# Kernel optimization log

Measured on AMD Instinct MI355X. Metric: run time of the kernel, lower is better.

Reference implementation:

```python
import jax, jax.numpy as jnp
import numpy as np

N = 20000   # nodes
E = 320000  # edges
NE = 2000   # entities
H = 4       # attention heads
D = 128     # hidden_dim (per-head out feats)
K = 10      # knn k


def _gat(h, src, dst, W, al, ar, Wr, relu):
    # h: [N, Fin]; W: [H*D, Fin]; al/ar: [H, D]; Wr: [H*D, Fin]
    feat = (h @ W.T).reshape(N, H, D)                      # [N,H,D]
    el = jnp.sum(feat * al[None], axis=-1)                 # [N,H]
    er = jnp.sum(feat * ar[None], axis=-1)                 # [N,H]
    e = jax.nn.leaky_relu(el[src] + er[dst], 0.2)          # [E,H]
    emax = jax.ops.segment_max(e, dst, num_segments=N)
    emax = jnp.where(jnp.isfinite(emax), emax, 0.0)
    a = jnp.exp(e - emax[dst])                             # [E,H]
    asum = jax.ops.segment_sum(a, dst, num_segments=N)
    asum = jnp.where(asum > 0, asum, 1.0)
    alpha = a / asum[dst]                                  # edge softmax over incoming edges
    msg = alpha[:, :, None] * feat[src]                    # [E,H,D]
    rst = jax.ops.segment_sum(msg, dst, num_segments=N)    # [N,H,D]
    rst = rst + (h @ Wr.T).reshape(N, H, D)                # residual
    if relu:
        rst = jax.nn.relu(rst)
    return rst


def _mlp2(x, W1, b1, W2, b2):
    return jax.nn.sigmoid(jax.nn.relu(x @ W1.T + b1) @ W2.T + b2)


def setup_inputs() -> dict:
    key = jax.random.key(0)
    ks = jax.random.split(key, 32)
    f32 = jnp.float32
    p = lambda i, s: (jax.random.normal(ks[i], s, dtype=f32) * 0.05)
    inp = {
        'position': jax.random.normal(ks[0], (N, 2), dtype=f32),
        'w_embed': jax.random.normal(ks[1], (N, 126), dtype=f32),
        'src': jax.random.randint(ks[2], (E,), 0, N),
        'dst': jax.random.randint(ks[3], (E,), 0, N),
        'entity': jax.random.randint(ks[4], (N,), 0, NE),
        # GAT layer 1 (in=128)
        'W1': p(5, (H * D, 128)), 'al1': p(6, (H, D)), 'ar1': p(7, (H, D)), 'Wr1': p(8, (H * D, 128)),
        # GAT layer 2 (in=512)
        'W2': p(9, (H * D, H * D)), 'al2': p(10, (H, D)), 'ar2': p(11, (H, D)), 'Wr2': p(12, (H * D, H * D)),
        # GAT layer 3 (in=512)
        'W3': p(13, (H * D, H * D)), 'al3': p(14, (H, D)), 'ar3': p(15, (H, D)), 'Wr3': p(16, (H * D, H * D)),
        # w_group_mlp
        'Wg1': p(17, (D, D)), 'bg1': p(18, (D,)), 'Wg2': p(19, (1, D)), 'bg2': p(20, (1,)),
        # entity_linear
        'We': p(21, (D, D)), 'be': p(22, (D,)),
        # entity_link_mlp
        'Wl1': p(23, (D, D)), 'bl1': p(24, (D,)), 'Wl2': p(25, (1, D)), 'bl2': p(26, (1,)),
        # entity_classify
        'Wc': p(27, (4, D)), 'bc': p(28, (4,)),
    }
    return inp


def reference(position, w_embed, src, dst, entity,
              W1, al1, ar1, Wr1, W2, al2, ar2, Wr2, W3, al3, ar3, Wr3,
              Wg1, bg1, Wg2, bg2, We, be, Wl1, bl1, Wl2, bl2, Wc, bc):
    h = jnp.concatenate([position, w_embed], axis=1)        # [N,128]
    h = _gat(h, src, dst, W1, al1, ar1, Wr1, True).reshape(N, H * D)
    h = _gat(h, src, dst, W2, al2, ar2, Wr2, True).reshape(N, H * D)
    h = _gat(h, src, dst, W3, al3, ar3, Wr3, False).mean(axis=1)  # [N,D]

    # pairwise group score over edges
    groups_score = _mlp2(jnp.abs(h[src] - h[dst]), Wg1, bg1, Wg2, bg2).squeeze(-1)  # [E]

    # per-entity segment reduce
    ent_sum = jax.ops.segment_sum(h, entity, num_segments=NE)            # [NE,D]
    entity_states = ent_sum @ We.T + be                                  # [NE,D]
    pos_sum = jax.ops.segment_sum(position, entity, num_segments=NE)     # [NE,2]
    cnt = jax.ops.segment_sum(jnp.ones((N,), jnp.float32), entity, num_segments=NE)
    entity_positions = pos_sum / jnp.maximum(cnt, 1.0)[:, None]          # [NE,2]

    # knn graph on entity centroids (k=10, includes self like dgl.knn_graph)
    d2 = jnp.sum((entity_positions[:, None, :] - entity_positions[None, :, :]) ** 2, axis=-1)  # [NE,NE]
    _, knn_idx = jax.lax.top_k(-d2, K)                                   # [NE,K]
    src_e = knn_idx.reshape(-1)                                          # [NE*K]
    dst_e = jnp.repeat(jnp.arange(NE), K)
    entity_link_score = _mlp2(jnp.abs(entity_states[src_e] - entity_states[dst_e]),
                              Wl1, bl1, Wl2, bl2).squeeze(-1)            # [NE*K]

    entity_class = jax.nn.sigmoid(entity_states @ Wc.T + bc)             # [NE,4]
    return (groups_score, entity_class, entity_positions, entity_link_score)
```

## Files before the change

### kernel.cpp

```cpp
#include <hip/hip_runtime.h>
#include <math.h>

#define N_NODES 20000
#define N_EDGES 320000
#define NENT    2000
#define KNN_K   10

typedef __attribute__((ext_vector_type(4))) float f32x4;
typedef __attribute__((ext_vector_type(8))) short bf16x8;
typedef __attribute__((ext_vector_type(8))) unsigned short u16x8;
typedef __attribute__((ext_vector_type(4))) unsigned short u16x4;

__device__ __forceinline__ unsigned short f2bf(float f) {
  union { float f; unsigned u; } v; v.f = f;
  unsigned r = v.u + 0x7fffu + ((v.u >> 16) & 1u);
  return (unsigned short)(r >> 16);
}
__device__ __forceinline__ float bf2f(unsigned short u) {
  union { unsigned u; float f; } v; v.u = ((unsigned)u) << 16;
  return v.f;
}
__device__ __forceinline__ float sigmoidf(float x) {
  return 1.f / (1.f + __expf(-x));
}
__device__ __forceinline__ void gload_lds16(const unsigned short* g, unsigned short* lds) {
  __builtin_amdgcn_global_load_lds(
      (const __attribute__((address_space(1))) unsigned int*)g,
      (__attribute__((address_space(3))) unsigned int*)lds, 16, 0, 0);
}

__global__ void k_build_h0(const float* __restrict__ pos, const float* __restrict__ wemb,
                           unsigned short* __restrict__ h0) {
  int i = blockIdx.x * blockDim.x + threadIdx.x;
  if (i >= N_NODES * 128) return;
  int n = i >> 7, c = i & 127;
  float v = (c < 2) ? pos[n * 2 + c] : wemb[n * 126 + (c - 2)];
  h0[i] = f2bf(v);
}

__global__ void k_f2bf(const float* __restrict__ in, unsigned short* __restrict__ out, int n) {
  int i = blockIdx.x * blockDim.x + threadIdx.x;
  if (i * 4 >= n) return;
  f32x4 v = *(const f32x4*)(in + i * 4);
  u16x4 o;
  o[0] = f2bf(v[0]); o[1] = f2bf(v[1]); o[2] = f2bf(v[2]); o[3] = f2bf(v[3]);
  *(u16x4*)(out + i * 4) = o;
}

__global__ __launch_bounds__(256) void k_gemm_bt(
    const unsigned short* __restrict__ A, const unsigned short* __restrict__ B,
    unsigned short* __restrict__ C, int M, int Nc, int K) {
  __shared__ __align__(16) unsigned short As[128 * 64];
  __shared__ __align__(16) unsigned short Bs[128 * 64];
  const int bm = blockIdx.x * 128, bn = blockIdx.y * 128;
  const int t = threadIdx.x;
  const int l = t & 63, w = t >> 6;
  const int wr = w >> 1, wc = w & 1;
  f32x4 acc[4][4];
#pragma unroll
  for (int m = 0; m < 4; ++m)
#pragma unroll
    for (int n = 0; n < 4; ++n) acc[m][n] = (f32x4){0.f, 0.f, 0.f, 0.f};

  for (int kb = 0; kb < K; kb += 64) {
    __syncthreads();
#pragma unroll
    for (int i = 0; i < 4; ++i) {
      int c = t + 256 * i;
      int row = c >> 3, cc = c & 7;
      int scc = cc ^ (row & 7);
      int ar = bm + row; if (ar > M - 1) ar = M - 1;
      gload_lds16(A + (size_t)ar * K + kb + scc * 8, &As[(size_t)(w * 64 + 256 * i) * 8]);
      gload_lds16(B + (size_t)(bn + row) * K + kb + scc * 8,
                  &Bs[(size_t)(w * 64 + 256 * i) * 8]);
    }
    __syncthreads();
#pragma unroll
    for (int kk = 0; kk < 2; ++kk) {
      bf16x8 af[4], bfr[4];
#pragma unroll
      for (int m = 0; m < 4; ++m) {
        int row = wr * 64 + m * 16 + (l & 15);
        int g = (kk * 4 + (l >> 4)) ^ (row & 7);
        af[m] = *(const bf16x8*)&As[row * 64 + g * 8];
      }
#pragma unroll
      for (int n = 0; n < 4; ++n) {
        int row = wc * 64 + n * 16 + (l & 15);
        int g = (kk * 4 + (l >> 4)) ^ (row & 7);
        bfr[n] = *(const bf16x8*)&Bs[row * 64 + g * 8];
      }
#pragma unroll
      for (int m = 0; m < 4; ++m)
#pragma unroll
        for (int n = 0; n < 4; ++n)
          acc[m][n] = __builtin_amdgcn_mfma_f32_16x16x32_bf16(af[m], bfr[n], acc[m][n], 0, 0, 0);
    }
  }
#pragma unroll
  for (int m = 0; m < 4; ++m) {
    int r0 = bm + wr * 64 + m * 16 + ((l >> 4) << 2);
#pragma unroll
    for (int n = 0; n < 4; ++n) {
      int c0 = bn + wc * 64 + n * 16 + (l & 15);
#pragma unroll
      for (int r = 0; r < 4; ++r) {
        int row = r0 + r;
        if (row < M) C[(size_t)row * Nc + c0] = f2bf(acc[m][n][r]);
      }
    }
  }
}

__global__ void k_el_er(const unsigned short* __restrict__ feat, int fstride,
                        const float* __restrict__ al, const float* __restrict__ ar,
                        float* __restrict__ el, float* __restrict__ er) {
  int wid = (blockIdx.x * blockDim.x + threadIdx.x) >> 6;
  if (wid >= N_NODES) return;
  int l = threadIdx.x & 63;
  int g = l >> 4, q = l & 15;
  u16x8 fv = *(const u16x8*)(feat + (size_t)wid * fstride + l * 8);
  const float* alp = al + g * 128 + q * 8;
  const float* arp = ar + g * 128 + q * 8;
  float sl = 0.f, sr = 0.f;
#pragma unroll
  for (int j = 0; j < 8; ++j) { float f = bf2f(fv[j]); sl += f * alp[j]; sr += f * arp[j]; }
#pragma unroll
  for (int d = 1; d < 16; d <<= 1) { sl += __shfl_xor(sl, d); sr += __shfl_xor(sr, d); }
  if (q == 0) { el[wid * 4 + g] = sl; er[wid * 4 + g] = sr; }
}

__global__ void k_hist(const int* __restrict__ dst, int* __restrict__ indeg) {
  int e = blockIdx.x * blockDim.x + threadIdx.x;
  if (e < N_EDGES) atomicAdd(&indeg[dst[e]], 1);
}

__global__ __launch_bounds__(1024) void k_scan_fast(const int* __restrict__ indeg,
                                                    int* __restrict__ indptr,
                                                    int* __restrict__ cursor) {
  __shared__ int wsum[16];
  const int t = threadIdx.x;
  const int l = t & 63, w = t >> 6;
  const int CH = 20;
  int base = t * CH;
  int vals[CH];
  int s = 0;
#pragma unroll
  for (int i = 0; i < CH; ++i) {
    int idx = base + i;
    int v = (idx < N_NODES) ? indeg[idx] : 0;
    vals[i] = v;
    s += v;
  }
  int ss = s;
#pragma unroll
  for (int d = 1; d < 64; d <<= 1) { int o = __shfl_up(ss, d); if (l >= d) ss += o; }
  if (l == 63) wsum[w] = ss;
  __syncthreads();
  if (t < 16) {
    int v = wsum[t];
#pragma unroll
    for (int d = 1; d < 16; d <<= 1) { int o = __shfl_up(v, d); if (t >= d) v += o; }
    wsum[t] = v;
  }
  __syncthreads();
  int run = ((w > 0) ? wsum[w - 1] : 0) + ss - s;
  if (t == 0) indptr[0] = 0;
#pragma unroll
  for (int i = 0; i < CH; ++i) {
    int idx = base + i;
    if (idx < N_NODES) {
      cursor[idx] = run;
      run += vals[i];
      indptr[idx + 1] = run;
    }
  }
}

__global__ void k_scatter(const int* __restrict__ src, const int* __restrict__ dst,
                          int* __restrict__ cursor, int* __restrict__ csr_src) {
  int e = blockIdx.x * blockDim.x + threadIdx.x;
  if (e < N_EDGES) {
    int p = atomicAdd(&cursor[dst[e]], 1);
    csr_src[p] = src[e];
  }
}

template <bool FINAL>
__global__ void k_gat_agg(const unsigned short* __restrict__ feat,
                          const unsigned short* __restrict__ hres, int fstride,
                          const float* __restrict__ el, const float* __restrict__ er,
                          const int* __restrict__ indptr, const int* __restrict__ csr_src,
                          unsigned short* __restrict__ hnext, float* __restrict__ h3,
                          unsigned short* __restrict__ h3b) {
  int wid = (blockIdx.x * blockDim.x + threadIdx.x) >> 6;
  if (wid >= N_NODES) return;
  int l = threadIdx.x & 63;
  int g = l >> 4;
  int beg = indptr[wid], end = indptr[wid + 1];
  f32x4 er4 = *(const f32x4*)(er + wid * 4);
  const float NI = -__builtin_inff();
  f32x4 mx = (f32x4){NI, NI, NI, NI};
  for (int j = beg + l; j < end; j += 64) {
    int s = csr_src[j];
    f32x4 el4 = *(const f32x4*)(el + s * 4);
#pragma unroll
    for (int h = 0; h < 4; ++h) {
      float v = el4[h] + er4[h];
      v = (v >= 0.f) ? v : 0.2f * v;
      mx[h] = fmaxf(mx[h], v);
    }
  }
#pragma unroll
  for (int d = 1; d < 64; d <<= 1) {
#pragma unroll
    for (int h = 0; h < 4; ++h) mx[h] = fmaxf(mx[h], __shfl_xor(mx[h], d));
  }
  float m_g = mx[g];
  float er_g = er4[g];
  float asum = 0.f;
  float acc[8];
#pragma unroll
  for (int j2 = 0; j2 < 8; ++j2) acc[j2] = 0.f;
  const unsigned short* fbase = feat + l * 8;
  int j = beg;
  for (; j + 4 <= end; j += 4) {
    int s0 = csr_src[j + 0], s1 = csr_src[j + 1];
    int s2 = csr_src[j + 2], s3 = csr_src[j + 3];
    float q0 = el[s0 * 4 + g], q1 = el[s1 * 4 + g];
    float q2 = el[s2 * 4 + g], q3 = el[s3 * 4 + g];
    u16x8 f0 = *(const u16x8*)(fbase + (size_t)s0 * fstride);
    u16x8 f1 = *(const u16x8*)(fbase + (size_t)s1 * fstride);
    u16x8 f2 = *(const u16x8*)(fbase + (size_t)s2 * fstride);
    u16x8 f3 = *(const u16x8*)(fbase + (size_t)s3 * fstride);
    float e0 = q0 + er_g; e0 = (e0 >= 0.f) ? e0 : 0.2f * e0;
    float e1 = q1 + er_g; e1 = (e1 >= 0.f) ? e1 : 0.2f * e1;
    float e2 = q2 + er_g; e2 = (e2 >= 0.f) ? e2 : 0.2f * e2;
    float e3 = q3 + er_g; e3 = (e3 >= 0.f) ? e3 : 0.2f * e3;
    float p0 = __expf(e0 - m_g), p1 = __expf(e1 - m_g);
    float p2 = __expf(e2 - m_g), p3 = __expf(e3 - m_g);
    asum += (p0 + p1) + (p2 + p3);
#pragma unroll
    for (int k = 0; k < 8; ++k)
      acc[k] += p0 * bf2f(f0[k]) + p1 * bf2f(f1[k]) + p2 * bf2f(f2[k]) + p3 * bf2f(f3[k]);
  }
  for (; j < end; ++j) {
    int s = csr_src[j];
    float ev = el[s * 4 + g] + er_g;
    ev = (ev >= 0.f) ? ev : 0.2f * ev;
    float p = __expf(ev - m_g);
    asum += p;
    u16x8 fv = *(const u16x8*)(fbase + (size_t)s * fstride);
#pragma unroll
    for (int k = 0; k < 8; ++k) acc[k] += p * bf2f(fv[k]);
  }
  float inv = (end > beg) ? 1.f / asum : 1.f;
  u16x8 hv = *(const u16x8*)(hres + (size_t)wid * fstride + l * 8);
  float o[8];
#pragma unroll
  for (int k = 0; k < 8; ++k) o[k] = acc[k] * inv + bf2f(hv[k]);
  if constexpr (!FINAL) {
    u16x8 ob;
#pragma unroll
    for (int k = 0; k < 8; ++k) ob[k] = f2bf(fmaxf(o[k], 0.f));
    *(u16x8*)(hnext + (size_t)wid * 512 + l * 8) = ob;
  } else {
#pragma unroll
    for (int k = 0; k < 8; ++k) {
      float v = o[k];
      v += __shfl_xor(v, 16);
      v += __shfl_xor(v, 32);
      o[k] = v * 0.25f;
    }
    if (g == 0) {
      f32x4 o0 = (f32x4){o[0], o[1], o[2], o[3]};
      f32x4 o1 = (f32x4){o[4], o[5], o[6], o[7]};
      *(f32x4*)(h3 + (size_t)wid * 128 + l * 8) = o0;
      *(f32x4*)(h3 + (size_t)wid * 128 + l * 8 + 4) = o1;
      u16x8 hb;
#pragma unroll
      for (int k = 0; k < 8; ++k) hb[k] = f2bf(o[k]);
      *(u16x8*)(h3b + (size_t)wid * 128 + l * 8) = hb;
    }
  }
}

template <int MODE>
__global__ __launch_bounds__(256) void k_pair_mlp(
    const unsigned short* __restrict__ X, const int* __restrict__ ia,
    const int* __restrict__ ib, const unsigned short* __restrict__ Wb,
    const float* __restrict__ b1, const float* __restrict__ W2,
    const float* __restrict__ b2, float* __restrict__ out, int npairs) {
  __shared__ __align__(16) unsigned short Xs[4][32 * 128];
  const int t = threadIdx.x;
  const int l = t & 63, w = t >> 6;
  unsigned short* xs = Xs[w];
  const int base = (blockIdx.x * 4 + w) * 32;
  {
    int e = base + (l >> 1);
    if (e >= npairs) e = npairs - 1;
    int sa, sb;
    if (MODE == 0) { sa = ia[e]; sb = ib[e]; }
    else           { sa = ia[e]; sb = e / KNN_K; }
    int hf = l & 1, el = l >> 1;
    const unsigned short* pa = X + (size_t)sa * 128 + hf * 64;
    const unsigned short* pb = X + (size_t)sb * 128 + hf * 64;
#pragma unroll
    for (int c = 0; c < 8; ++c) {
      u16x8 av = *(const u16x8*)(pa + c * 8);
      u16x8 bv = *(const u16x8*)(pb + c * 8);
      u16x8 xv;
#pragma unroll
      for (int j = 0; j < 8; ++j) xv[j] = f2bf(fabsf(bf2f(av[j]) - bf2f(bv[j])));
      int sg = (hf * 8 + c) ^ (el & 15);
      *(u16x8*)&xs[el * 128 + sg * 8] = xv;
    }
  }
  __syncthreads();
  bf16x8 af[2][4];
#pragma unroll
  for (int m = 0; m < 2; ++m)
#pragma unroll
    for (int kk = 0; kk < 4; ++kk) {
      int row = m * 16 + (l & 15);
      int sg = (kk * 4 + (l >> 4)) ^ (row & 15);
      af[m][kk] = *(const bf16x8*)&xs[row * 128 + sg * 8];
    }
  const size_t wlane = (size_t)(l & 15) * 128 + (l >> 4) * 8;
  bf16x8 bcur[4], bnext[4];
#pragma unroll
  for (int kk = 0; kk < 4; ++kk)
    bcur[kk] = *(const bf16x8*)(Wb + wlane + kk * 32);
  float part[2][4];
#pragma unroll
  for (int m = 0; m < 2; ++m)
#pragma unroll
    for (int r = 0; r < 4; ++r) part[m][r] = 0.f;
#pragma unroll
  for (int n = 0; n < 8; ++n) {
    if (n < 7) {
#pragma unroll
      for (int kk = 0; kk < 4; ++kk)
        bnext[kk] = *(const bf16x8*)(Wb + wlane + (size_t)(n + 1) * 2048 + kk * 32);
    }
    f32x4 acc0 = (f32x4){0.f, 0.f, 0.f, 0.f};
    f32x4 acc1 = (f32x4){0.f, 0.f, 0.f, 0.f};
#pragma unroll
    for (int kk = 0; kk < 4; ++kk) {
      acc0 = __builtin_amdgcn_mfma_f32_16x16x32_bf16(af[0][kk], bcur[kk], acc0, 0, 0, 0);
      acc1 = __builtin_amdgcn_mfma_f32_16x16x32_bf16(af[1][kk], bcur[kk], acc1, 0, 0, 0);
    }
    int col = n * 16 + (l & 15);
    float bb = b1[col], w2v = W2[col];
#pragma unroll
    for (int r = 0; r < 4; ++r) {
      part[0][r] += fmaxf(acc0[r] + bb, 0.f) * w2v;
      part[1][r] += fmaxf(acc1[r] + bb, 0.f) * w2v;
    }
#pragma unroll
    for (int kk = 0; kk < 4; ++kk) bcur[kk] = bnext[kk];
  }
#pragma unroll
  for (int d = 1; d < 16; d <<= 1)
#pragma unroll
    for (int m = 0; m < 2; ++m)
#pragma unroll
      for (int r = 0; r < 4; ++r) part[m][r] += __shfl_xor(part[m][r], d);
  if ((l & 15) == 0) {
    int q = l >> 4;
    float b2v = b2[0];
#pragma unroll
    for (int m = 0; m < 2; ++m) {
      int e = base + m * 16 + q * 4;
      f32x4 ov;
#pragma unroll
      for (int r = 0; r < 4; ++r) ov[r] = sigmoidf(part[m][r] + b2v);
      if (e + 3 < npairs) *(f32x4*)(out + e) = ov;
      else {
#pragma unroll
        for (int r = 0; r < 4; ++r) if (e + r < npairs) out[e + r] = ov[r];
      }
    }
  }
}

__global__ void k_ent_scatter(const float* __restrict__ h3, const float* __restrict__ pos,
                              const int* __restrict__ entity, float* __restrict__ ent_sum,
                              float* __restrict__ pos_sum, float* __restrict__ cnt) {
  int i = blockIdx.x * blockDim.x + threadIdx.x;
  if (i >= N_NODES * 32) return;
  int n = i >> 5, c = i & 31;
  int e = entity[n];
  f32x4 v = *(const f32x4*)(h3 + (size_t)n * 128 + c * 4);
  atomicAdd(&ent_sum[e * 128 + c * 4 + 0], v[0]);
  atomicAdd(&ent_sum[e * 128 + c * 4 + 1], v[1]);
  atomicAdd(&ent_sum[e * 128 + c * 4 + 2], v[2]);
  atomicAdd(&ent_sum[e * 128 + c * 4 + 3], v[3]);
  if (c == 0) {
    atomicAdd(&pos_sum[e * 2 + 0], pos[n * 2 + 0]);
    atomicAdd(&pos_sum[e * 2 + 1], pos[n * 2 + 1]);
    atomicAdd(&cnt[e], 1.f);
  }
}

__global__ void k_entity_states(const float* __restrict__ ent_sum, const float* __restrict__ We,
                                const float* __restrict__ be, float* __restrict__ es) {
  int i = blockIdx.x * blockDim.x + threadIdx.x;
  if (i >= NENT * 128) return;
  int e = i >> 7, j = i & 127;
  const float* x = ent_sum + (size_t)e * 128;
  const float* wrow = We + (size_t)j * 128;
  float s = be[j];
  for (int k = 0; k < 128; k += 4) {
    f32x4 xv = *(const f32x4*)(x + k);
    f32x4 wv = *(const f32x4*)(wrow + k);
    s += xv[0] * wv[0] + xv[1] * wv[1] + xv[2] * wv[2] + xv[3] * wv[3];
  }
  es[i] = s;
}

__global__ void k_entity_class(const float* __restrict__ es, const float* __restrict__ Wc,
                               const float* __restrict__ bc, float* __restrict__ out) {
  int i = blockIdx.x * blockDim.x + threadIdx.x;
  if (i >= NENT * 4) return;
  int e = i >> 2, c = i & 3;
  const float* x = es + (size_t)e * 128;
  const float* wrow = Wc + (size_t)c * 128;
  float s = bc[c];
  for (int k = 0; k < 128; ++k) s += x[k] * wrow[k];
  out[i] = sigmoidf(s);
}

__global__ void k_entity_pos(const float* __restrict__ pos_sum, const float* __restrict__ cnt,
                             float* __restrict__ outpos, float* __restrict__ wspos) {
  int e = blockIdx.x * blockDim.x + threadIdx.x;
  if (e >= NENT) return;
  float c = fmaxf(cnt[e], 1.f);
  float x = pos_sum[e * 2] / c, y = pos_sum[e * 2 + 1] / c;
  outpos[e * 2] = x; outpos[e * 2 + 1] = y;
  wspos[e * 2] = x; wspos[e * 2 + 1] = y;
}

__global__ __launch_bounds__(256) void k_knn(const float* __restrict__ entpos,
                                             int* __restrict__ knn) {
  __shared__ float d2row[NENT];
  __shared__ float rv[256];
  __shared__ int ri[256];
  int i = blockIdx.x, t = threadIdx.x;
  float px = entpos[i * 2], py = entpos[i * 2 + 1];
  for (int j = t; j < NENT; j += 256) {
    float dx = px - entpos[j * 2], dy = py - entpos[j * 2 + 1];
    d2row[j] = __fadd_rn(__fmul_rn(dx, dx), __fmul_rn(dy, dy));
  }
  __syncthreads();
  for (int k = 0; k < KNN_K; ++k) {
    float bv = __builtin_inff(); int bi = 0x7fffffff;
    for (int j = t; j < NENT; j += 256) {
      float v = d2row[j];
      if (v < bv) { bv = v; bi = j; }
    }
    rv[t] = bv; ri[t] = bi;
    __syncthreads();
    for (int s = 128; s > 0; s >>= 1) {
      if (t < s) {
        if (rv[t + s] < rv[t] || (rv[t + s] == rv[t] && ri[t + s] < ri[t])) {
          rv[t] = rv[t + s]; ri[t] = ri[t + s];
        }
      }
      __syncthreads();
    }
    if (t == 0) { knn[i * KNN_K + k] = ri[0]; d2row[ri[0]] = __builtin_inff(); }
    __syncthreads();
  }
}

extern "C" void kernel_launch(void* const* d_in, const int* in_sizes, int n_in,
                              void* d_out, int out_size, void* d_ws, size_t ws_size,
                              hipStream_t stream) {
  const float* position = (const float*)d_in[0];
  const float* w_embed  = (const float*)d_in[1];
  const int*   src      = (const int*)d_in[2];
  const int*   dst      = (const int*)d_in[3];
  const int*   entity   = (const int*)d_in[4];
  const float* W1 = (const float*)d_in[5];
  const float* al1 = (const float*)d_in[6];
  const float* ar1 = (const float*)d_in[7];
  const float* Wr1 = (const float*)d_in[8];
  const float* W2 = (const float*)d_in[9];
  const float* al2 = (const float*)d_in[10];
  const float* ar2 = (const float*)d_in[11];
  const float* Wr2 = (const float*)d_in[12];
  const float* W3 = (const float*)d_in[13];
  const float* al3 = (const float*)d_in[14];
  const float* ar3 = (const float*)d_in[15];
  const float* Wr3 = (const float*)d_in[16];
  const float* Wg1 = (const float*)d_in[17];
  const float* bg1 = (const float*)d_in[18];
  const float* Wg2 = (const float*)d_in[19];
  const float* bg2 = (const float*)d_in[20];
  const float* We  = (const float*)d_in[21];
  const float* be  = (const float*)d_in[22];
  const float* Wl1 = (const float*)d_in[23];
  const float* bl1 = (const float*)d_in[24];
  const float* Wl2 = (const float*)d_in[25];
  const float* bl2 = (const float*)d_in[26];
  const float* Wc  = (const float*)d_in[27];
  const float* bc  = (const float*)d_in[28];

  float* out_groups = (float*)d_out;
  float* out_class  = out_groups + N_EDGES;
  float* out_pos    = out_class + NENT * 4;
  float* out_link   = out_pos + NENT * 2;

  char* ws = (char*)d_ws;
  size_t off = 0;
  auto carve = [&](size_t bytes) -> char* {
    char* p = ws + off;
    off = (off + bytes + 255) & ~(size_t)255;
    return p;
  };
  unsigned short* featC = (unsigned short*)carve((size_t)N_NODES * 1024 * 2);
  unsigned short* hA = (unsigned short*)carve((size_t)N_NODES * 512 * 2);
  unsigned short* hB = (unsigned short*)carve((size_t)N_NODES * 512 * 2);
  unsigned short* wbf = (unsigned short*)carve((size_t)1024 * 512 * 2);
  unsigned short* wg1b = (unsigned short*)carve(128 * 128 * 2);
  unsigned short* wl1b = (unsigned short*)carve(128 * 128 * 2);
  float* el = (float*)carve((size_t)N_NODES * 4 * 4);
  float* er = (float*)carve((size_t)N_NODES * 4 * 4);
  int* indeg = (int*)carve((size_t)N_NODES * 4);
  int* indptr = (int*)carve((size_t)(N_NODES + 1) * 4);
  int* cursor = (int*)carve((size_t)N_NODES * 4);
  int* csr_src = (int*)carve((size_t)N_EDGES * 4);
  float* h3 = (float*)carve((size_t)N_NODES * 128 * 4);
  unsigned short* h3b = (unsigned short*)carve((size_t)N_NODES * 128 * 2);
  float* ent_sum = (float*)carve((size_t)NENT * 128 * 4);
  float* pos_sum = (float*)carve((size_t)NENT * 2 * 4);
  float* cnt = (float*)carve((size_t)NENT * 4);
  float* es = (float*)carve((size_t)NENT * 128 * 4);
  unsigned short* esb = (unsigned short*)carve((size_t)NENT * 128 * 2);
  float* wspos = (float*)carve((size_t)NENT * 2 * 4);
  int* knn = (int*)carve((size_t)NENT * KNN_K * 4);

  hipMemsetAsync(indeg, 0, (size_t)N_NODES * 4, stream);
  k_hist<<<(N_EDGES + 255) / 256, 256, 0, stream>>>(dst, indeg);
  k_scan_fast<<<1, 1024, 0, stream>>>(indeg, indptr, cursor);
  k_scatter<<<(N_EDGES + 255) / 256, 256, 0, stream>>>(src, dst, cursor, csr_src);

  k_build_h0<<<(N_NODES * 128 + 255) / 256, 256, 0, stream>>>(position, w_embed, hA);

  dim3 ggrid((N_NODES + 127) / 128, 8), gblk(256);

  k_f2bf<<<(512 * 128 / 4 + 255) / 256, 256, 0, stream>>>(W1, wbf, 512 * 128);
  k_f2bf<<<(512 * 128 / 4 + 255) / 256, 256, 0, stream>>>(Wr1, wbf + 512 * 128, 512 * 128);
  k_gemm_bt<<<ggrid, gblk, 0, stream>>>(hA, wbf, featC, N_NODES, 1024, 128);
  k_el_er<<<5000, 256, 0, stream>>>(featC, 1024, al1, ar1, el, er);
  k_gat_agg<false><<<5000, 256, 0, stream>>>(featC, featC + 512, 1024, el, er, indptr,
                                             csr_src, hB, nullptr, nullptr);

  k_f2bf<<<(512 * 512 / 4 + 255) / 256, 256, 0, stream>>>(W2, wbf, 512 * 512);
  k_f2bf<<<(512 * 512 / 4 + 255) / 256, 256, 0, stream>>>(Wr2, wbf + 512 * 512, 512 * 512);
  k_gemm_bt<<<ggrid, gblk, 0, stream>>>(hB, wbf, featC, N_NODES, 1024, 512);
  k_el_er<<<5000, 256, 0, stream>>>(featC, 1024, al2, ar2, el, er);
  k_gat_agg<false><<<5000, 256, 0, stream>>>(featC, featC + 512, 1024, el, er, indptr,
                                             csr_src, hA, nullptr, nullptr);

  k_f2bf<<<(512 * 512 / 4 + 255) / 256, 256, 0, stream>>>(W3, wbf, 512 * 512);
  k_f2bf<<<(512 * 512 / 4 + 255) / 256, 256, 0, stream>>>(Wr3, wbf + 512 * 512, 512 * 512);
  k_gemm_bt<<<ggrid, gblk, 0, stream>>>(hA, wbf, featC, N_NODES, 1024, 512);
  k_el_er<<<5000, 256, 0, stream>>>(featC, 1024, al3, ar3, el, er);
  k_gat_agg<true><<<5000, 256, 0, stream>>>(featC, featC + 512, 1024, el, er, indptr,
                                            csr_src, nullptr, h3, h3b);

  k_f2bf<<<(128 * 128 / 4 + 255) / 256, 256, 0, stream>>>(Wg1, wg1b, 128 * 128);
  k_pair_mlp<0><<<N_EDGES / 128, 256, 0, stream>>>(h3b, src, dst, wg1b, bg1, Wg2, bg2,
                                                   out_groups, N_EDGES);

  hipMemsetAsync(ent_sum, 0, (size_t)NENT * 128 * 4, stream);
  hipMemsetAsync(pos_sum, 0, (size_t)NENT * 2 * 4, stream);
  hipMemsetAsync(cnt, 0, (size_t)NENT * 4, stream);
  k_ent_scatter<<<(N_NODES * 32 + 255) / 256, 256, 0, stream>>>(h3, position, entity, ent_sum,
                                                                pos_sum, cnt);
  k_entity_states<<<(NENT * 128 + 255) / 256, 256, 0, stream>>>(ent_sum, We, be, es);
  k_entity_class<<<(NENT * 4 + 255) / 256, 256, 0, stream>>>(es, Wc, bc, out_class);
  k_entity_pos<<<(NENT + 255) / 256, 256, 0, stream>>>(pos_sum, cnt, out_pos, wspos);
  k_knn<<<NENT, 256, 0, stream>>>(wspos, knn);
  k_f2bf<<<(NENT * 128 / 4 + 255) / 256, 256, 0, stream>>>(es, esb, NENT * 128);
  k_f2bf<<<(128 * 128 / 4 + 255) / 256, 256, 0, stream>>>(Wl1, wl1b, 128 * 128);
  k_pair_mlp<1><<<(NENT * KNN_K / 32 + 3) / 4, 256, 0, stream>>>(esb, knn, nullptr, wl1b, bl1,
                                                                 Wl2, bl2, out_link,
                                                                 NENT * KNN_K);
}
```

Before: 511.7 us.

## Stage pair-MLP weights in LDS and gather edge features directly into MFMA fragments

The pair MLP kernel no longer stages the |a-b| edge features through shared memory. Each lane now loads its MFMA A-fragment straight from global memory. The 128x128 weight matrix is pre-swizzled on the host side of the pipeline by a new conversion kernel and copied once per block into LDS with direct global-to-LDS loads, instead of every wave streaming it from global/L2 with register double buffering. This is meant to cut redundant weight traffic and the LDS round trip for features. The cost is a 32KB LDS footprint per block, which may limit occupancy.

```diff
diff --git a/kernel.cpp b/kernel.cpp
--- a/kernel.cpp
+++ b/kernel.cpp
@@ -45,6 +45,14 @@
   u16x4 o;
   o[0] = f2bf(v[0]); o[1] = f2bf(v[1]); o[2] = f2bf(v[2]); o[3] = f2bf(v[3]);
   *(u16x4*)(out + i * 4) = o;
+}
+
+__global__ void k_f2bf_wswz(const float* __restrict__ in, unsigned short* __restrict__ out) {
+  int i = blockIdx.x * blockDim.x + threadIdx.x;
+  if (i >= 128 * 128) return;
+  int row = i >> 7, k = i & 127;
+  int sg = (k >> 3) ^ (row & 15);
+  out[row * 128 + sg * 8 + (k & 7)] = f2bf(in[i]);
 }
 
 __global__ __launch_bounds__(256) void k_gemm_bt(
@@ -288,77 +296,64 @@
 template <int MODE>
 __global__ __launch_bounds__(256) void k_pair_mlp(
     const unsigned short* __restrict__ X, const int* __restrict__ ia,
-    const int* __restrict__ ib, const unsigned short* __restrict__ Wb,
+    const int* __restrict__ ib, const unsigned short* __restrict__ WbSwz,
     const float* __restrict__ b1, const float* __restrict__ W2,
     const float* __restrict__ b2, float* __restrict__ out, int npairs) {
-  __shared__ __align__(16) unsigned short Xs[4][32 * 128];
+  __shared__ __align__(16) unsigned short Ws[128 * 128];
   const int t = threadIdx.x;
   const int l = t & 63, w = t >> 6;
-  unsigned short* xs = Xs[w];
-  const int base = (blockIdx.x * 4 + w) * 32;
-  {
-    int e = base + (l >> 1);
-    if (e >= npairs) e = npairs - 1;
+#pragma unroll
+  for (int i = 0; i < 8; ++i)
+    gload_lds16(WbSwz + i * 2048 + w * 512 + l * 8, &Ws[i * 2048 + w * 512]);
+  const int base = blockIdx.x * 128 + w * 32;
+  bf16x8 af[2][4];
+#pragma unroll
+  for (int m = 0; m < 2; ++m) {
+    int e = base + m * 16 + (l & 15);
+    if (MODE == 1 && e >= npairs) e = npairs - 1;
     int sa, sb;
     if (MODE == 0) { sa = ia[e]; sb = ib[e]; }
     else           { sa = ia[e]; sb = e / KNN_K; }
-    int hf = l & 1, el = l >> 1;
-    const unsigned short* pa = X + (size_t)sa * 128 + hf * 64;
-    const unsigned short* pb = X + (size_t)sb * 128 + hf * 64;
-#pragma unroll
-    for (int c = 0; c < 8; ++c) {
-      u16x8 av = *(const u16x8*)(pa + c * 8);
-      u16x8 bv = *(const u16x8*)(pb + c * 8);
+    const unsigned short* pa = X + (size_t)sa * 128 + (l >> 4) * 8;
+    const unsigned short* pb = X + (size_t)sb * 128 + (l >> 4) * 8;
+#pragma unroll
+    for (int kk = 0; kk < 4; ++kk) {
+      u16x8 av = *(const u16x8*)(pa + kk * 32);
+      u16x8 bv = *(const u16x8*)(pb + kk * 32);
       u16x8 xv;
 #pragma unroll
       for (int j = 0; j < 8; ++j) xv[j] = f2bf(fabsf(bf2f(av[j]) - bf2f(bv[j])));
-      int sg = (hf * 8 + c) ^ (el & 15);
-      *(u16x8*)&xs[el * 128 + sg * 8] = xv;
+      af[m][kk] = *(bf16x8*)&xv;
     }
   }
   __syncthreads();
-  bf16x8 af[2][4];
+  float part[2][4];
 #pragma unroll
   for (int m = 0; m < 2; ++m)
 #pragma unroll
+    for (int r = 0; r < 4; ++r) part[m][r] = 0.f;
+#pragma unroll
+  for (int n = 0; n < 8; ++n) {
+    int rowv = n * 16 + (l & 15);
+    bf16x8 bfr[4];
+#pragma unroll
     for (int kk = 0; kk < 4; ++kk) {
-      int row = m * 16 + (l & 15);
-      int sg = (kk * 4 + (l >> 4)) ^ (row & 15);
-      af[m][kk] = *(const bf16x8*)&xs[row * 128 + sg * 8];
-    }
-  const size_t wlane = (size_t)(l & 15) * 128 + (l >> 4) * 8;
-  bf16x8 bcur[4], bnext[4];
-#pragma unroll
-  for (int kk = 0; kk < 4; ++kk)
-    bcur[kk] = *(const bf16x8*)(Wb + wlane + kk * 32);
-  float part[2][4];
-#pragma unroll
-  for (int m = 0; m < 2; ++m)
-#pragma unroll
-    for (int r = 0; r < 4; ++r) part[m][r] = 0.f;
-#pragma unroll
-  for (int n = 0; n < 8; ++n) {
-    if (n < 7) {
-#pragma unroll
-      for (int kk = 0; kk < 4; ++kk)
-        bnext[kk] = *(const bf16x8*)(Wb + wlane + (size_t)(n + 1) * 2048 + kk * 32);
+      int sg = (kk * 4 + (l >> 4)) ^ (rowv & 15);
+      bfr[kk] = *(const bf16x8*)&Ws[rowv * 128 + sg * 8];
     }
     f32x4 acc0 = (f32x4){0.f, 0.f, 0.f, 0.f};
     f32x4 acc1 = (f32x4){0.f, 0.f, 0.f, 0.f};
 #pragma unroll
     for (int kk = 0; kk < 4; ++kk) {
-      acc0 = __builtin_amdgcn_mfma_f32_16x16x32_bf16(af[0][kk], bcur[kk], acc0, 0, 0, 0);
-      acc1 = __builtin_amdgcn_mfma_f32_16x16x32_bf16(af[1][kk], bcur[kk], acc1, 0, 0, 0);
-    }
-    int col = n * 16 + (l & 15);
-    float bb = b1[col], w2v = W2[col];
+      acc0 = __builtin_amdgcn_mfma_f32_16x16x32_bf16(af[0][kk], bfr[kk], acc0, 0, 0, 0);
+      acc1 = __builtin_amdgcn_mfma_f32_16x16x32_bf16(af[1][kk], bfr[kk], acc1, 0, 0, 0);
+    }
+    float bb = b1[rowv], w2v = W2[rowv];
 #pragma unroll
     for (int r = 0; r < 4; ++r) {
       part[0][r] += fmaxf(acc0[r] + bb, 0.f) * w2v;
       part[1][r] += fmaxf(acc1[r] + bb, 0.f) * w2v;
     }
-#pragma unroll
-    for (int kk = 0; kk < 4; ++kk) bcur[kk] = bnext[kk];
   }
 #pragma unroll
   for (int d = 1; d < 16; d <<= 1)
@@ -571,7 +566,7 @@
   k_gat_agg<true><<<5000, 256, 0, stream>>>(featC, featC + 512, 1024, el, er, indptr,
                                             csr_src, nullptr, h3, h3b);
 
-  k_f2bf<<<(128 * 128 / 4 + 255) / 256, 256, 0, stream>>>(Wg1, wg1b, 128 * 128);
+  k_f2bf_wswz<<<(128 * 128 + 255) / 256, 256, 0, stream>>>(Wg1, wg1b);
   k_pair_mlp<0><<<N_EDGES / 128, 256, 0, stream>>>(h3b, src, dst, wg1b, bg1, Wg2, bg2,
                                                    out_groups, N_EDGES);
 
@@ -585,8 +580,8 @@
   k_entity_pos<<<(NENT + 255) / 256, 256, 0, stream>>>(pos_sum, cnt, out_pos, wspos);
   k_knn<<<NENT, 256, 0, stream>>>(wspos, knn);
   k_f2bf<<<(NENT * 128 / 4 + 255) / 256, 256, 0, stream>>>(es, esb, NENT * 128);
-  k_f2bf<<<(128 * 128 / 4 + 255) / 256, 256, 0, stream>>>(Wl1, wl1b, 128 * 128);
-  k_pair_mlp<1><<<(NENT * KNN_K / 32 + 3) / 4, 256, 0, stream>>>(esb, knn, nullptr, wl1b, bl1,
-                                                                 Wl2, bl2, out_link,
-                                                                 NENT * KNN_K);
-}
+  k_f2bf_wswz<<<(128 * 128 + 255) / 256, 256, 0, stream>>>(Wl1, wl1b);
+  k_pair_mlp<1><<<(NENT * KNN_K + 127) / 128, 256, 0, stream>>>(esb, knn, nullptr, wl1b, bl1,
+                                                                Wl2, bl2, out_link,
+                                                                NENT * KNN_K);
+}
```

Result: faster. 475.0 us (-7.2%).
